# Kernel optimization log

Hardware: AMD Instinct MI355X
Metric: run time of the kernel (lower is better)

Reference implementation:

```python
import jax, jax.numpy as jnp
import numpy as np

BATCH = 8192
FEATURES = 8192
INITIAL_SPARSITY_RATE = 0.5


def setup_inputs() -> dict:
    key = jax.random.key(0)
    k1, _ = jax.random.split(key)
    inputs = jax.random.normal(k1, (BATCH, FEATURES), dtype=jnp.float32)
    # trainable scalar weight, shape (1,), constant-initialized
    sparsity_rate = jnp.full((1,), INITIAL_SPARSITY_RATE, dtype=jnp.float32)
    return {"inputs": inputs, "sparsity_rate": sparsity_rate}


def reference(inputs, sparsity_rate):
    # inputs: [B, F]; sparsity_rate: [1]
    n = inputs.shape[-1]
    # descending sort along feature axis
    sorted_desc = -jnp.sort(-inputs, axis=-1)
    # per-call threshold index (integer cast, non-differentiable like TF's tf.cast)
    rate = jnp.clip(sparsity_rate[0], 0.0, 1.0)
    idx = jax.lax.stop_gradient((rate * jnp.float32(n)).astype(jnp.int32))
    thresh = jnp.take(sorted_desc, idx, axis=-1)           # [B]: value at rank `idx`
    max_in = jnp.max(inputs, axis=-1)                      # [B]
    t_r = max_in - thresh                                  # [B]
    # relu-masked weights: relu(x + t_r - max) == relu(x - thresh)
    w_t = jax.nn.relu(inputs + t_r[:, None] - max_in[:, None])
    weighted_exp = w_t * jnp.exp(inputs)                   # [B, F]
    sum_we = jnp.sum(weighted_exp, axis=-1, keepdims=True)
    return weighted_exp / sum_we
```

## Files before the change

### kernel.cpp

```cpp
#include <hip/hip_runtime.h>

#define ROWS 8192
#define COLS 8192
#define TPB  512
#define EPT  16
#define VPT  4
#define NW   8

__device__ __forceinline__ unsigned f2k(float x) {
    unsigned u = __float_as_uint(x);
    return (u & 0x80000000u) ? ~u : (u | 0x80000000u);
}
__device__ __forceinline__ float k2f(unsigned k) {
    unsigned u = (k & 0x80000000u) ? (k & 0x7FFFFFFFu) : ~k;
    return __uint_as_float(u);
}

__global__ __launch_bounds__(TPB, 8)
void rsoftmax_kernel(const float* __restrict__ in,
                     const float* __restrict__ rate_p,
                     float* __restrict__ out)
{
    const int t    = threadIdx.x;
    const int lane = t & 63;
    const int wave = t >> 6;
    const int row  = blockIdx.x;
    const float4* in4  = (const float4*)(in  + (size_t)row * COLS);
    float4*       out4 = (float4*)      (out + (size_t)row * COLS);

    unsigned key[EPT];
    #pragma unroll
    for (int j = 0; j < VPT; ++j) {
        float4 v = in4[t + j * TPB];
        key[4*j+0] = f2k(v.x);
        key[4*j+1] = f2k(v.y);
        key[4*j+2] = f2k(v.z);
        key[4*j+3] = f2k(v.w);
    }
    #pragma unroll
    for (int j = 0; j < EPT; ++j) asm volatile("" : "+v"(key[j]));

    float rate = rate_p[0];
    rate = fminf(fmaxf(rate, 0.0f), 1.0f);
    int idx = (int)(rate * (float)COLS);
    if (idx > COLS - 1) idx = COLS - 1;
    if (idx < 0) idx = 0;

    __shared__ unsigned sHistW[NW][256];
    __shared__ unsigned sWaveTot[4];
    __shared__ unsigned sK, sPfx;
    __shared__ float    sSum[NW];
    __shared__ float    sInv;

    if (t == 0) { sK = (unsigned)(idx + 1); sPfx = 0u; }

    #pragma unroll
    for (int pass = 0; pass < 4; ++pass) {
        const int      s      = 24 - 8 * pass;
        const unsigned himask = (pass == 0) ? 0u : (0xFFFFFFFFu << (s + 8));

        __syncthreads();
        const unsigned pfx = sPfx;
        const unsigned kk  = sK;

        #pragma unroll
        for (int i = 0; i < 4; ++i) sHistW[wave][lane + 64*i] = 0u;

        #pragma unroll
        for (int j = 0; j < EPT; ++j) {
            if (((key[j] ^ pfx) & himask) == 0u)
                atomicAdd(&sHistW[wave][(key[j] >> s) & 0xFFu], 1u);
        }
        __syncthreads();

        unsigned h = 0, v = 0;
        if (t < 256) {
            #pragma unroll
            for (int w = 0; w < NW; ++w) h += sHistW[w][t];

            v = h;
            #pragma unroll
            for (int off = 1; off < 64; off <<= 1) {
                unsigned u = __shfl_down(v, off, 64);
                v += (lane + off < 64) ? u : 0u;
            }
            if (lane == 0) sWaveTot[wave] = v;
        }
        __syncthreads();

        if (t < 256) {
            unsigned above = 0u;
            #pragma unroll
            for (int w = 0; w < 4; ++w)
                if (w > wave) above += sWaveTot[w];

            const unsigned st = v + above;
            const unsigned sn = st - h;
            if (st >= kk && sn < kk) {
                sPfx = pfx | ((unsigned)t << s);
                sK   = kk - sn;
            }
        }
    }
    __syncthreads();
    const float thr = k2f(sPfx);

    float lsum = 0.0f;
    #pragma unroll
    for (int j = 0; j < EPT; ++j) {
        float x = k2f(key[j]);
        lsum += fmaxf(x - thr, 0.0f) * __expf(x);
    }
    #pragma unroll
    for (int off = 32; off > 0; off >>= 1)
        lsum += __shfl_down(lsum, off, 64);
    if (lane == 0) sSum[wave] = lsum;
    __syncthreads();
    if (t == 0) {
        float s = 0.0f;
        #pragma unroll
        for (int w = 0; w < NW; ++w) s += sSum[w];
        sInv = 1.0f / s;
    }
    __syncthreads();
    const float inv = sInv;

    #pragma unroll
    for (int j = 0; j < VPT; ++j) {
        float4 o;
        float x0 = k2f(key[4*j+0]); o.x = fmaxf(x0 - thr, 0.0f) * __expf(x0) * inv;
        float x1 = k2f(key[4*j+1]); o.y = fmaxf(x1 - thr, 0.0f) * __expf(x1) * inv;
        float x2 = k2f(key[4*j+2]); o.z = fmaxf(x2 - thr, 0.0f) * __expf(x2) * inv;
        float x3 = k2f(key[4*j+3]); o.w = fmaxf(x3 - thr, 0.0f) * __expf(x3) * inv;
        out4[t + j * TPB] = o;
    }
}

extern "C" void kernel_launch(void* const* d_in, const int* in_sizes, int n_in,
                              void* d_out, int out_size, void* d_ws, size_t ws_size,
                              hipStream_t stream)
{
    const float* in   = (const float*)d_in[0];
    const float* rate = (const float*)d_in[1];
    float*       out  = (float*)d_out;
    rsoftmax_kernel<<<dim3(ROWS), dim3(TPB), 0, stream>>>(in, rate, out);
}
```

Baseline: 464.9 us.

## Process four rows per block with next-row prefetch and lighter LDS barriers

Each block now handles four consecutive rows, loading the next row's float4 data into registers while the current row runs its radix-select passes and normalization. This aims to hide global load latency behind the histogram and reduction work. Plain __syncthreads calls are also swapped for a custom barrier that waits only on LDS counters, so outstanding global prefetches are not drained. The trade-offs are a quarter as many blocks, extra registers held for the prefetch buffer, and a longer serial loop inside each block.

```diff
diff --git a/kernel.cpp b/kernel.cpp
--- a/kernel.cpp
+++ b/kernel.cpp
@@ -6,6 +6,8 @@
 #define EPT  16
 #define VPT  4
 #define NW   8
+#define RPB  4
+#define GRID (ROWS / RPB)
 
 __device__ __forceinline__ unsigned f2k(float x) {
     unsigned u = __float_as_uint(x);
@@ -16,6 +18,14 @@
     return __uint_as_float(u);
 }
 
+__device__ __forceinline__ void bar_lds() {
+    __builtin_amdgcn_sched_barrier(0);
+    asm volatile("s_waitcnt lgkmcnt(0)" ::: "memory");
+    __builtin_amdgcn_sched_barrier(0);
+    __builtin_amdgcn_s_barrier();
+    __builtin_amdgcn_sched_barrier(0);
+}
+
 __global__ __launch_bounds__(TPB, 8)
 void rsoftmax_kernel(const float* __restrict__ in,
                      const float* __restrict__ rate_p,
@@ -24,27 +34,6 @@
     const int t    = threadIdx.x;
     const int lane = t & 63;
     const int wave = t >> 6;
-    const int row  = blockIdx.x;
-    const float4* in4  = (const float4*)(in  + (size_t)row * COLS);
-    float4*       out4 = (float4*)      (out + (size_t)row * COLS);
-
-    unsigned key[EPT];
-    #pragma unroll
-    for (int j = 0; j < VPT; ++j) {
-        float4 v = in4[t + j * TPB];
-        key[4*j+0] = f2k(v.x);
-        key[4*j+1] = f2k(v.y);
-        key[4*j+2] = f2k(v.z);
-        key[4*j+3] = f2k(v.w);
-    }
-    #pragma unroll
-    for (int j = 0; j < EPT; ++j) asm volatile("" : "+v"(key[j]));
-
-    float rate = rate_p[0];
-    rate = fminf(fmaxf(rate, 0.0f), 1.0f);
-    int idx = (int)(rate * (float)COLS);
-    if (idx > COLS - 1) idx = COLS - 1;
-    if (idx < 0) idx = 0;
 
     __shared__ unsigned sHistW[NW][256];
     __shared__ unsigned sWaveTot[4];
@@ -52,87 +41,117 @@
     __shared__ float    sSum[NW];
     __shared__ float    sInv;
 
-    if (t == 0) { sK = (unsigned)(idx + 1); sPfx = 0u; }
+    float rate = rate_p[0];
+    rate = fminf(fmaxf(rate, 0.0f), 1.0f);
+    int idx = (int)(rate * (float)COLS);
+    if (idx > COLS - 1) idx = COLS - 1;
+    if (idx < 0) idx = 0;
+    const unsigned k0 = (unsigned)(idx + 1);
 
-    #pragma unroll
-    for (int pass = 0; pass < 4; ++pass) {
-        const int      s      = 24 - 8 * pass;
-        const unsigned himask = (pass == 0) ? 0u : (0xFFFFFFFFu << (s + 8));
+    const size_t row0 = (size_t)blockIdx.x * RPB;
 
-        __syncthreads();
-        const unsigned pfx = sPfx;
-        const unsigned kk  = sK;
+    float4 pf[VPT];
+    {
+        const float4* p = (const float4*)(in + row0 * COLS);
+        #pragma unroll
+        for (int j = 0; j < VPT; ++j) pf[j] = p[t + j * TPB];
+    }
+
+    for (int r = 0; r < RPB; ++r) {
+        unsigned key[EPT];
+        #pragma unroll
+        for (int j = 0; j < VPT; ++j) {
+            float4 v = pf[j];
+            key[4*j+0] = f2k(v.x); key[4*j+1] = f2k(v.y);
+            key[4*j+2] = f2k(v.z); key[4*j+3] = f2k(v.w);
+        }
+        if (r + 1 < RPB) {
+            const float4* p = (const float4*)(in + (row0 + r + 1) * COLS);
+            #pragma unroll
+            for (int j = 0; j < VPT; ++j) pf[j] = p[t + j * TPB];
+        }
+        #pragma unroll
+        for (int j = 0; j < EPT; ++j) asm volatile("" : "+v"(key[j]));
+
+        if (t == 0) { sK = k0; sPfx = 0u; }
 
         #pragma unroll
-        for (int i = 0; i < 4; ++i) sHistW[wave][lane + 64*i] = 0u;
+        for (int pass = 0; pass < 4; ++pass) {
+            const int      s      = 24 - 8 * pass;
+            const unsigned himask = (pass == 0) ? 0u : (0xFFFFFFFFu << (s + 8));
 
+            bar_lds();
+            const unsigned pfx = sPfx;
+            const unsigned kk  = sK;
+
+            #pragma unroll
+            for (int i = 0; i < 4; ++i) sHistW[wave][lane + 64*i] = 0u;
+
+            #pragma unroll
+            for (int j = 0; j < EPT; ++j) {
+                if (((key[j] ^ pfx) & himask) == 0u)
+                    atomicAdd(&sHistW[wave][(key[j] >> s) & 0xFFu], 1u);
+            }
+            bar_lds();
+
+            unsigned h = 0, v = 0;
+            if (t < 256) {
+                #pragma unroll
+                for (int w = 0; w < NW; ++w) h += sHistW[w][t];
+                v = h;
+                #pragma unroll
+                for (int off = 1; off < 64; off <<= 1) {
+                    unsigned u = __shfl_down(v, off, 64);
+                    v += (lane + off < 64) ? u : 0u;
+                }
+                if (lane == 0) sWaveTot[wave] = v;
+            }
+            bar_lds();
+            if (t < 256) {
+                unsigned above = 0u;
+                #pragma unroll
+                for (int w = 0; w < 4; ++w) if (w > wave) above += sWaveTot[w];
+                const unsigned st = v + above;
+                const unsigned sn = st - h;
+                if (st >= kk && sn < kk) {
+                    sPfx = pfx | ((unsigned)t << s);
+                    sK   = kk - sn;
+                }
+            }
+        }
+        bar_lds();
+        const float thr = k2f(sPfx);
+
+        float lsum = 0.0f;
         #pragma unroll
         for (int j = 0; j < EPT; ++j) {
-            if (((key[j] ^ pfx) & himask) == 0u)
-                atomicAdd(&sHistW[wave][(key[j] >> s) & 0xFFu], 1u);
+            float x = k2f(key[j]);
+            lsum += fmaxf(x - thr, 0.0f) * __expf(x);
         }
-        __syncthreads();
+        #pragma unroll
+        for (int off = 32; off > 0; off >>= 1)
+            lsum += __shfl_down(lsum, off, 64);
+        if (lane == 0) sSum[wave] = lsum;
+        bar_lds();
+        if (t == 0) {
+            float ssum = 0.0f;
+            #pragma unroll
+            for (int w = 0; w < NW; ++w) ssum += sSum[w];
+            sInv = 1.0f / ssum;
+        }
+        bar_lds();
+        const float inv = sInv;
 
-        unsigned h = 0, v = 0;
-        if (t < 256) {
-            #pragma unroll
-            for (int w = 0; w < NW; ++w) h += sHistW[w][t];
-
-            v = h;
-            #pragma unroll
-            for (int off = 1; off < 64; off <<= 1) {
-                unsigned u = __shfl_down(v, off, 64);
-                v += (lane + off < 64) ? u : 0u;
-            }
-            if (lane == 0) sWaveTot[wave] = v;
+        float4* out4 = (float4*)(out + (row0 + r) * COLS);
+        #pragma unroll
+        for (int j = 0; j < VPT; ++j) {
+            float4 o;
+            float x0 = k2f(key[4*j+0]); o.x = fmaxf(x0 - thr, 0.0f) * __expf(x0) * inv;
+            float x1 = k2f(key[4*j+1]); o.y = fmaxf(x1 - thr, 0.0f) * __expf(x1) * inv;
+            float x2 = k2f(key[4*j+2]); o.z = fmaxf(x2 - thr, 0.0f) * __expf(x2) * inv;
+            float x3 = k2f(key[4*j+3]); o.w = fmaxf(x3 - thr, 0.0f) * __expf(x3) * inv;
+            out4[t + j * TPB] = o;
         }
-        __syncthreads();
-
-        if (t < 256) {
-            unsigned above = 0u;
-            #pragma unroll
-            for (int w = 0; w < 4; ++w)
-                if (w > wave) above += sWaveTot[w];
-
-            const unsigned st = v + above;
-            const unsigned sn = st - h;
-            if (st >= kk && sn < kk) {
-                sPfx = pfx | ((unsigned)t << s);
-                sK   = kk - sn;
-            }
-        }
-    }
-    __syncthreads();
-    const float thr = k2f(sPfx);
-
-    float lsum = 0.0f;
-    #pragma unroll
-    for (int j = 0; j < EPT; ++j) {
-        float x = k2f(key[j]);
-        lsum += fmaxf(x - thr, 0.0f) * __expf(x);
-    }
-    #pragma unroll
-    for (int off = 32; off > 0; off >>= 1)
-        lsum += __shfl_down(lsum, off, 64);
-    if (lane == 0) sSum[wave] = lsum;
-    __syncthreads();
-    if (t == 0) {
-        float s = 0.0f;
-        #pragma unroll
-        for (int w = 0; w < NW; ++w) s += sSum[w];
-        sInv = 1.0f / s;
-    }
-    __syncthreads();
-    const float inv = sInv;
-
-    #pragma unroll
-    for (int j = 0; j < VPT; ++j) {
-        float4 o;
-        float x0 = k2f(key[4*j+0]); o.x = fmaxf(x0 - thr, 0.0f) * __expf(x0) * inv;
-        float x1 = k2f(key[4*j+1]); o.y = fmaxf(x1 - thr, 0.0f) * __expf(x1) * inv;
-        float x2 = k2f(key[4*j+2]); o.z = fmaxf(x2 - thr, 0.0f) * __expf(x2) * inv;
-        float x3 = k2f(key[4*j+3]); o.w = fmaxf(x3 - thr, 0.0f) * __expf(x3) * inv;
-        out4[t + j * TPB] = o;
     }
 }
 
@@ -143,5 +162,5 @@
     const float* in   = (const float*)d_in[0];
     const float* rate = (const float*)d_in[1];
     float*       out  = (float*)d_out;
-    rsoftmax_kernel<<<dim3(ROWS), dim3(TPB), 0, stream>>>(in, rate, out);
+    rsoftmax_kernel<<<dim3(GRID), dim3(TPB), 0, stream>>>(in, rate, out);
 }
```

Result: slower. 486.2 us (+4.6%).
